# Optimization experiments

Measured on AMD Instinct MI355X. Metric: run time of the kernel, lower is better.

Reference implementation:

```python
import jax, jax.numpy as jnp
import numpy as np

B, T, S, H = 8, 256, 256, 512

def setup_inputs() -> dict:
    key = jax.random.key(0)
    k1, k2, k3, k4, k5, k6 = jax.random.split(key, 6)
    query = jax.random.normal(k1, (B, T, H), dtype=jnp.float32)
    encoder_outputs = jax.random.normal(k2, (B, S, H), dtype=jnp.float32)
    # lengths in [1, S] so every row has at least one valid source position
    src_lengths = jax.random.randint(k3, (B,), 1, S + 1, dtype=jnp.int64)
    scale = 1.0 / np.sqrt(H)
    W_h = jax.random.normal(k4, (H, H), dtype=jnp.float32) * scale  # nn.Linear weight (out, in)
    W_s = jax.random.normal(k5, (H, H), dtype=jnp.float32) * scale
    v = jax.random.normal(k6, (H,), dtype=jnp.float32) * scale     # nn.Linear(H,1) weight squeezed
    return {"query": query, "encoder_outputs": encoder_outputs,
            "src_lengths": src_lengths, "W_h": W_h, "W_s": W_s, "v": v}

def reference(query, encoder_outputs, src_lengths, W_h, W_s, v):
    # Linear without bias: y = x @ W^T
    enc_f = jnp.einsum('bsh,oh->bso', encoder_outputs, W_h)   # (B,S,H)
    qry_f = jnp.einsum('bth,oh->bto', query, W_s)             # (B,T,H)
    # additive score: v^T tanh(enc_f + qry_f), broadcast over (T,S)
    scores = jnp.einsum('btsh,h->bts',
                        jnp.tanh(enc_f[:, None, :, :] + qry_f[:, :, None, :]), v)  # (B,T,S)
    mask = jnp.arange(S)[None, :] >= src_lengths[:, None]      # (B,S) True = pad
    scores = jnp.where(mask[:, None, :], -jnp.inf, scores)
    attn_weights = jax.nn.softmax(scores, axis=-1)             # (B,T,S)
    attn_out = jnp.einsum('bts,bsh->bth', attn_weights, encoder_outputs)
    return attn_out
```

## Files before the change

### kernel.cpp

```cpp
#include <hip/hip_runtime.h>
#include <cstddef>
#include <math.h>

#define BD 8
#define TD 256
#define SD 256
#define HD 512
#define K2F 2.885390081777927f

#define EXP2(x) __builtin_amdgcn_exp2f(x)
#define RCP(x)  __builtin_amdgcn_rcpf(x)

typedef __attribute__((ext_vector_type(8))) short short8;
typedef __attribute__((ext_vector_type(4))) float float4v;
typedef unsigned short u16;

__device__ __forceinline__ u16 bf_hi(float x) {
    union { float f; unsigned u; } v; v.f = x;
    unsigned r = v.u + 0x7fff + ((v.u >> 16) & 1);
    return (u16)(r >> 16);
}
__device__ __forceinline__ float bf_tof(u16 h) {
    union { float f; unsigned u; } v; v.u = ((unsigned)h) << 16;
    return v.f;
}
__device__ __forceinline__ float exp2_sat(float x) {
    return EXP2(fminf(fmaxf(x, -80.0f), 80.0f));
}

__global__ __launch_bounds__(256) void convert_kernel(
    const float* __restrict__ enc, const float* __restrict__ qry,
    const float* __restrict__ Wh,  const float* __restrict__ Ws,
    u16* __restrict__ Ah, u16* __restrict__ Al,
    u16* __restrict__ Bh, u16* __restrict__ Bl)
{
    const int bid = blockIdx.x, tid = threadIdx.x;
    const float* src; u16 *dh, *dl; size_t i4;
    if (bid < 1024)      { src = enc; dh = Ah;                    dl = Al;                    i4 = (size_t)bid * 256 + tid; }
    else if (bid < 2048) { src = qry; dh = Ah + (size_t)2048*512; dl = Al + (size_t)2048*512; i4 = (size_t)(bid-1024)*256 + tid; }
    else if (bid < 2304) { src = Wh;  dh = Bh;                    dl = Bl;                    i4 = (size_t)(bid-2048)*256 + tid; }
    else                 { src = Ws;  dh = Bh + (size_t)512*512;  dl = Bl + (size_t)512*512;  i4 = (size_t)(bid-2304)*256 + tid; }
    float4 x = ((const float4*)src)[i4];
    u16 h0 = bf_hi(x.x), h1 = bf_hi(x.y), h2 = bf_hi(x.z), h3 = bf_hi(x.w);
    ushort4 hv = make_ushort4(h0, h1, h2, h3);
    ushort4 lv = make_ushort4(bf_hi(x.x - bf_tof(h0)), bf_hi(x.y - bf_tof(h1)),
                              bf_hi(x.z - bf_tof(h2)), bf_hi(x.w - bf_tof(h3)));
    ((ushort4*)dh)[i4] = hv;
    ((ushort4*)dl)[i4] = lv;
}

#define LSTR 40
__global__ __launch_bounds__(256) void proj_kernel(
    const u16* __restrict__ Ahg, const u16* __restrict__ Alg,
    const u16* __restrict__ Bhg, const u16* __restrict__ Blg,
    float* __restrict__ encT, float* __restrict__ qryf)
{
    __shared__ u16 LAh[64*LSTR], LAl[64*LSTR], LBh[64*LSTR], LBl[64*LSTR];

    const int tid = threadIdx.x;
    const int l = tid & 63, w = tid >> 6;
    const int rf = l & 15, q = l >> 4;
    const int my = blockIdx.y;
    const bool isq = my >= 32;
    const int m0 = my * 64;
    const int n0 = blockIdx.x * 64;
    const int brow0 = (isq ? 512 : 0) + n0;

    const int srow = tid >> 2;
    const int scol = (tid & 3) * 8;
    const u16* pAh = Ahg + (size_t)(m0 + srow) * HD + scol;
    const u16* pAl = Alg + (size_t)(m0 + srow) * HD + scol;
    const u16* pBh = Bhg + (size_t)(brow0 + srow) * HD + scol;
    const u16* pBl = Blg + (size_t)(brow0 + srow) * HD + scol;

    const int mi = (w & 1) * 32, ni = (w >> 1) * 32;

    float4v acc[2][2] = {{{0,0,0,0},{0,0,0,0}},{{0,0,0,0},{0,0,0,0}}};

    short8 rah = *(const short8*)pAh;
    short8 ral = *(const short8*)pAl;
    short8 rbh = *(const short8*)pBh;
    short8 rbl = *(const short8*)pBl;

    for (int ks = 0; ks < 16; ++ks) {
        if (ks) __syncthreads();
        *(short8*)&LAh[srow * LSTR + scol] = rah;
        *(short8*)&LAl[srow * LSTR + scol] = ral;
        *(short8*)&LBh[srow * LSTR + scol] = rbh;
        *(short8*)&LBl[srow * LSTR + scol] = rbl;
        __syncthreads();
        if (ks + 1 < 16) {
            const int ko = (ks + 1) * 32;
            rah = *(const short8*)(pAh + ko);
            ral = *(const short8*)(pAl + ko);
            rbh = *(const short8*)(pBh + ko);
            rbl = *(const short8*)(pBl + ko);
        }
        short8 ah[2], al[2], bh[2], bl[2];
        #pragma unroll
        for (int i = 0; i < 2; ++i) {
            ah[i] = *(const short8*)&LAh[(mi + i * 16 + rf) * LSTR + q * 8];
            al[i] = *(const short8*)&LAl[(mi + i * 16 + rf) * LSTR + q * 8];
            bh[i] = *(const short8*)&LBh[(ni + i * 16 + rf) * LSTR + q * 8];
            bl[i] = *(const short8*)&LBl[(ni + i * 16 + rf) * LSTR + q * 8];
        }
        #pragma unroll
        for (int i = 0; i < 2; ++i)
            #pragma unroll
            for (int j = 0; j < 2; ++j) {
                acc[i][j] = __builtin_amdgcn_mfma_f32_16x16x32_bf16(ah[i], bh[j], acc[i][j], 0, 0, 0);
                acc[i][j] = __builtin_amdgcn_mfma_f32_16x16x32_bf16(ah[i], bl[j], acc[i][j], 0, 0, 0);
                acc[i][j] = __builtin_amdgcn_mfma_f32_16x16x32_bf16(al[i], bh[j], acc[i][j], 0, 0, 0);
            }
    }

    if (!isq) {
        const int b  = m0 >> 8;
        const int sb = (m0 & 255) + mi + q * 4;
        float* base = encT + (size_t)b * HD * SD;
        #pragma unroll
        for (int i = 0; i < 2; ++i)
            #pragma unroll
            for (int j = 0; j < 2; ++j) {
                float4 o = make_float4(exp2_sat(acc[i][j][0]*K2F), exp2_sat(acc[i][j][1]*K2F),
                                       exp2_sat(acc[i][j][2]*K2F), exp2_sat(acc[i][j][3]*K2F));
                *(float4*)(base + (size_t)(n0 + ni + j * 16 + rf) * SD + sb + i * 16) = o;
            }
    } else {
        const int mrow = (m0 - 2048) + mi + q * 4;
        #pragma unroll
        for (int i = 0; i < 2; ++i)
            #pragma unroll
            for (int j = 0; j < 2; ++j)
                #pragma unroll
                for (int r = 0; r < 4; ++r)
                    qryf[(size_t)(mrow + i * 16 + r) * HD + n0 + ni + j * 16 + rf] =
                        exp2_sat(acc[i][j][r] * K2F);
    }
}

__global__ __launch_bounds__(512) void attn_kernel(
    const float* __restrict__ enc,
    const float* __restrict__ encT,
    const float* __restrict__ qry_f,
    const float* __restrict__ v,
    const int*   __restrict__ lens,
    float* __restrict__ out)
{
    __shared__ float qls[HD * 4];
    __shared__ float pls[8 * 4 * 256];
    __shared__ float wls[4 * SD];

    const int blk = blockIdx.x;
    const int b   = blk >> 6;
    const int t0  = (blk & 63) * 4;
    const int tid = threadIdx.x;
    const int w   = tid >> 6;
    const int l   = tid & 63;

    {
        const float* qf = qry_f + ((size_t)b * TD + t0) * HD;
        float4 qv;
        qv.x = qf[0 * HD + tid]; qv.y = qf[1 * HD + tid];
        qv.z = qf[2 * HD + tid]; qv.w = qf[3 * HD + tid];
        *(float4*)&qls[tid * 4] = qv;
    }
    __syncthreads();

    float a[4][4];
    #pragma unroll
    for (int t = 0; t < 4; ++t)
        #pragma unroll
        for (int c = 0; c < 4; ++c) a[t][c] = 0.0f;
    {
        const float* ep = encT + (size_t)b * HD * SD + (size_t)(w * 64) * SD + l * 4;
        const int jbase = w * 64;
        #pragma unroll 4
        for (int jj = 0; jj < 64; ++jj) {
            float4 e = *(const float4*)(ep + (size_t)jj * SD);
            float4 q4 = *(const float4*)&qls[(jbase + jj) * 4];
            float vj = v[jbase + jj];
            float ev[4] = {e.x, e.y, e.z, e.w};
            float qv[4] = {q4.x, q4.y, q4.z, q4.w};
            #pragma unroll
            for (int t = 0; t < 4; ++t)
                #pragma unroll
                for (int c = 0; c < 4; ++c) {
                    float p = fmaf(ev[c], qv[t], 1.0f);
                    a[t][c] = fmaf(vj, RCP(p), a[t][c]);
                }
        }
    }
    #pragma unroll
    for (int t = 0; t < 4; ++t)
        *(float4*)&pls[(w * 4 + t) * 256 + l * 4] = make_float4(a[t][0], a[t][1], a[t][2], a[t][3]);
    __syncthreads();

    if (w < 4) {
        const int t = w;
        float p[4] = {0, 0, 0, 0};
        #pragma unroll
        for (int g = 0; g < 8; ++g) {
            float4 pp = *(const float4*)&pls[(g * 4 + t) * 256 + l * 4];
            p[0] += pp.x; p[1] += pp.y; p[2] += pp.z; p[3] += pp.w;
        }
        const int len = lens[b];
        const int s0 = l * 4;
        float sc[4];
        #pragma unroll
        for (int c = 0; c < 4; ++c)
            sc[c] = (s0 + c < len) ? -2.0f * p[c] : -INFINITY;
        float mx = fmaxf(fmaxf(sc[0], sc[1]), fmaxf(sc[2], sc[3]));
        #pragma unroll
        for (int off = 32; off; off >>= 1) mx = fmaxf(mx, __shfl_xor(mx, off));
        float ex[4]; float sum = 0.0f;
        #pragma unroll
        for (int c = 0; c < 4; ++c) { ex[c] = __expf(sc[c] - mx); sum += ex[c]; }
        #pragma unroll
        for (int off = 32; off; off >>= 1) sum += __shfl_xor(sum, off);
        const float inv = RCP(sum);
        *(float4*)&wls[t * SD + s0] = make_float4(ex[0]*inv, ex[1]*inv, ex[2]*inv, ex[3]*inv);
    }
    __syncthreads();

    const int g  = tid >> 7;
    const int h4 = (tid & 127) * 4;
    float* avred = pls;
    {
        const float* eb = enc + (size_t)b * SD * HD + h4;
        float4 o[4] = {{0,0,0,0},{0,0,0,0},{0,0,0,0},{0,0,0,0}};
        #pragma unroll 2
        for (int ss = 0; ss < 64; ++ss) {
            const int s = g * 64 + ss;
            float4 evv = *(const float4*)(eb + (size_t)s * HD);
            float wt[4];
            #pragma unroll
            for (int t = 0; t < 4; ++t) wt[t] = wls[t * SD + s];
            #pragma unroll
            for (int t = 0; t < 4; ++t) {
                o[t].x = fmaf(wt[t], evv.x, o[t].x);
                o[t].y = fmaf(wt[t], evv.y, o[t].y);
                o[t].z = fmaf(wt[t], evv.z, o[t].z);
                o[t].w = fmaf(wt[t], evv.w, o[t].w);
            }
        }
        #pragma unroll
        for (int t = 0; t < 4; ++t)
            *(float4*)&avred[(size_t)(g * 4 + t) * 512 + h4] = o[t];
    }
    __syncthreads();

    {
        const int t  = tid >> 7;
        const int hh = (tid & 127) * 4;
        float4 r = {0, 0, 0, 0};
        #pragma unroll
        for (int gg = 0; gg < 4; ++gg) {
            float4 x = *(const float4*)&avred[(size_t)(gg * 4 + t) * 512 + hh];
            r.x += x.x; r.y += x.y; r.z += x.z; r.w += x.w;
        }
        *(float4*)(out + ((size_t)b * TD + t0 + t) * HD + hh) = r;
    }
}

extern "C" void kernel_launch(void* const* d_in, const int* in_sizes, int n_in,
                              void* d_out, int out_size, void* d_ws, size_t ws_size,
                              hipStream_t stream) {
    const float* query = (const float*)d_in[0];
    const float* enc   = (const float*)d_in[1];
    const int*   lens  = (const int*)d_in[2];
    const float* W_h   = (const float*)d_in[3];
    const float* W_s   = (const float*)d_in[4];
    const float* v     = (const float*)d_in[5];
    float* out = (float*)d_out;

    char* ws = (char*)d_ws;
    float* encT = (float*)(ws);
    float* qryf = (float*)(ws + ((size_t)4  << 20));
    u16*   Ah   = (u16*)  (ws + ((size_t)8  << 20));
    u16*   Al   = (u16*)  (ws + ((size_t)12 << 20));
    u16*   Bh   = (u16*)  (ws + ((size_t)16 << 20));
    u16*   Bl   = (u16*)  (ws + ((size_t)17 << 20));

    convert_kernel<<<2560, 256, 0, stream>>>(enc, query, W_h, W_s, Ah, Al, Bh, Bl);

    dim3 pgrid(HD / 64, 64);
    proj_kernel<<<pgrid, 256, 0, stream>>>(Ah, Al, Bh, Bl, encT, qryf);

    attn_kernel<<<BD * (TD / 4), 512, 0, stream>>>(enc, encT, qryf, v, lens, out);
}
```

Baseline: 128.8 us.

## Replace split-bf16 projection with single fp16 MFMA and fuse conversion into GEMM

Drops the separate convert kernel and the hi/lo bf16 split: the projection GEMM now loads fp32 inputs directly, converts them to fp16 in registers and runs one f16 MFMA per tile instead of three bf16 MFMAs. This removes a kernel launch, the workspace round trip and two thirds of the MFMA work. The cost is lower precision, since fp16 has an 11-bit mantissa versus roughly 16 bits for the hi/lo split, and fp16 has limited range. The attention loop also software-prefetches the next encT row and changes its unroll, which reads one row past the end of each 64-row slice.

```diff
diff --git a/kernel.cpp b/kernel.cpp
--- a/kernel.cpp
+++ b/kernel.cpp
@@ -11,51 +11,20 @@
 #define EXP2(x) __builtin_amdgcn_exp2f(x)
 #define RCP(x)  __builtin_amdgcn_rcpf(x)
 
-typedef __attribute__((ext_vector_type(8))) short short8;
+typedef __attribute__((ext_vector_type(8))) _Float16 half8;
 typedef __attribute__((ext_vector_type(4))) float float4v;
-typedef unsigned short u16;
-
-__device__ __forceinline__ u16 bf_hi(float x) {
-    union { float f; unsigned u; } v; v.f = x;
-    unsigned r = v.u + 0x7fff + ((v.u >> 16) & 1);
-    return (u16)(r >> 16);
-}
-__device__ __forceinline__ float bf_tof(u16 h) {
-    union { float f; unsigned u; } v; v.u = ((unsigned)h) << 16;
-    return v.f;
-}
+
 __device__ __forceinline__ float exp2_sat(float x) {
     return EXP2(fminf(fmaxf(x, -80.0f), 80.0f));
 }
 
-__global__ __launch_bounds__(256) void convert_kernel(
+#define LSTR 40
+__global__ __launch_bounds__(256) void proj_kernel(
     const float* __restrict__ enc, const float* __restrict__ qry,
     const float* __restrict__ Wh,  const float* __restrict__ Ws,
-    u16* __restrict__ Ah, u16* __restrict__ Al,
-    u16* __restrict__ Bh, u16* __restrict__ Bl)
-{
-    const int bid = blockIdx.x, tid = threadIdx.x;
-    const float* src; u16 *dh, *dl; size_t i4;
-    if (bid < 1024)      { src = enc; dh = Ah;                    dl = Al;                    i4 = (size_t)bid * 256 + tid; }
-    else if (bid < 2048) { src = qry; dh = Ah + (size_t)2048*512; dl = Al + (size_t)2048*512; i4 = (size_t)(bid-1024)*256 + tid; }
-    else if (bid < 2304) { src = Wh;  dh = Bh;                    dl = Bl;                    i4 = (size_t)(bid-2048)*256 + tid; }
-    else                 { src = Ws;  dh = Bh + (size_t)512*512;  dl = Bl + (size_t)512*512;  i4 = (size_t)(bid-2304)*256 + tid; }
-    float4 x = ((const float4*)src)[i4];
-    u16 h0 = bf_hi(x.x), h1 = bf_hi(x.y), h2 = bf_hi(x.z), h3 = bf_hi(x.w);
-    ushort4 hv = make_ushort4(h0, h1, h2, h3);
-    ushort4 lv = make_ushort4(bf_hi(x.x - bf_tof(h0)), bf_hi(x.y - bf_tof(h1)),
-                              bf_hi(x.z - bf_tof(h2)), bf_hi(x.w - bf_tof(h3)));
-    ((ushort4*)dh)[i4] = hv;
-    ((ushort4*)dl)[i4] = lv;
-}
-
-#define LSTR 40
-__global__ __launch_bounds__(256) void proj_kernel(
-    const u16* __restrict__ Ahg, const u16* __restrict__ Alg,
-    const u16* __restrict__ Bhg, const u16* __restrict__ Blg,
     float* __restrict__ encT, float* __restrict__ qryf)
 {
-    __shared__ u16 LAh[64*LSTR], LAl[64*LSTR], LBh[64*LSTR], LBl[64*LSTR];
+    __shared__ _Float16 LA[64 * LSTR], LB[64 * LSTR];
 
     const int tid = threadIdx.x;
     const int l = tid & 63, w = tid >> 6;
@@ -64,54 +33,53 @@
     const bool isq = my >= 32;
     const int m0 = my * 64;
     const int n0 = blockIdx.x * 64;
-    const int brow0 = (isq ? 512 : 0) + n0;
 
     const int srow = tid >> 2;
     const int scol = (tid & 3) * 8;
-    const u16* pAh = Ahg + (size_t)(m0 + srow) * HD + scol;
-    const u16* pAl = Alg + (size_t)(m0 + srow) * HD + scol;
-    const u16* pBh = Bhg + (size_t)(brow0 + srow) * HD + scol;
-    const u16* pBl = Blg + (size_t)(brow0 + srow) * HD + scol;
+    const float* Abase = isq
+        ? qry + (size_t)(m0 - 2048 + srow) * HD + scol
+        : enc + (size_t)(m0 + srow) * HD + scol;
+    const float* Bbase = (isq ? Ws : Wh) + (size_t)(n0 + srow) * HD + scol;
 
     const int mi = (w & 1) * 32, ni = (w >> 1) * 32;
 
     float4v acc[2][2] = {{{0,0,0,0},{0,0,0,0}},{{0,0,0,0},{0,0,0,0}}};
 
-    short8 rah = *(const short8*)pAh;
-    short8 ral = *(const short8*)pAl;
-    short8 rbh = *(const short8*)pBh;
-    short8 rbl = *(const short8*)pBl;
+    float4 a0 = *(const float4*)(Abase);
+    float4 a1 = *(const float4*)(Abase + 4);
+    float4 b0 = *(const float4*)(Bbase);
+    float4 b1 = *(const float4*)(Bbase + 4);
 
     for (int ks = 0; ks < 16; ++ks) {
         if (ks) __syncthreads();
-        *(short8*)&LAh[srow * LSTR + scol] = rah;
-        *(short8*)&LAl[srow * LSTR + scol] = ral;
-        *(short8*)&LBh[srow * LSTR + scol] = rbh;
-        *(short8*)&LBl[srow * LSTR + scol] = rbl;
+        {
+            float af[8] = {a0.x,a0.y,a0.z,a0.w,a1.x,a1.y,a1.z,a1.w};
+            float bf[8] = {b0.x,b0.y,b0.z,b0.w,b1.x,b1.y,b1.z,b1.w};
+            half8 ha, hb;
+            #pragma unroll
+            for (int i = 0; i < 8; ++i) { ha[i] = (_Float16)af[i]; hb[i] = (_Float16)bf[i]; }
+            *(half8*)&LA[srow * LSTR + scol] = ha;
+            *(half8*)&LB[srow * LSTR + scol] = hb;
+        }
         __syncthreads();
         if (ks + 1 < 16) {
             const int ko = (ks + 1) * 32;
-            rah = *(const short8*)(pAh + ko);
-            ral = *(const short8*)(pAl + ko);
-            rbh = *(const short8*)(pBh + ko);
-            rbl = *(const short8*)(pBl + ko);
-        }
-        short8 ah[2], al[2], bh[2], bl[2];
+            a0 = *(const float4*)(Abase + ko);
+            a1 = *(const float4*)(Abase + ko + 4);
+            b0 = *(const float4*)(Bbase + ko);
+            b1 = *(const float4*)(Bbase + ko + 4);
+        }
+        half8 ah[2], bh[2];
         #pragma unroll
         for (int i = 0; i < 2; ++i) {
-            ah[i] = *(const short8*)&LAh[(mi + i * 16 + rf) * LSTR + q * 8];
-            al[i] = *(const short8*)&LAl[(mi + i * 16 + rf) * LSTR + q * 8];
-            bh[i] = *(const short8*)&LBh[(ni + i * 16 + rf) * LSTR + q * 8];
-            bl[i] = *(const short8*)&LBl[(ni + i * 16 + rf) * LSTR + q * 8];
+            ah[i] = *(const half8*)&LA[(mi + i * 16 + rf) * LSTR + q * 8];
+            bh[i] = *(const half8*)&LB[(ni + i * 16 + rf) * LSTR + q * 8];
         }
         #pragma unroll
         for (int i = 0; i < 2; ++i)
             #pragma unroll
-            for (int j = 0; j < 2; ++j) {
-                acc[i][j] = __builtin_amdgcn_mfma_f32_16x16x32_bf16(ah[i], bh[j], acc[i][j], 0, 0, 0);
-                acc[i][j] = __builtin_amdgcn_mfma_f32_16x16x32_bf16(ah[i], bl[j], acc[i][j], 0, 0, 0);
-                acc[i][j] = __builtin_amdgcn_mfma_f32_16x16x32_bf16(al[i], bh[j], acc[i][j], 0, 0, 0);
-            }
+            for (int j = 0; j < 2; ++j)
+                acc[i][j] = __builtin_amdgcn_mfma_f32_16x16x32_f16(ah[i], bh[j], acc[i][j], 0, 0, 0);
     }
 
     if (!isq) {
@@ -175,9 +143,10 @@
     {
         const float* ep = encT + (size_t)b * HD * SD + (size_t)(w * 64) * SD + l * 4;
         const int jbase = w * 64;
-        #pragma unroll 4
+        float4 e = *(const float4*)ep;
+        #pragma unroll 2
         for (int jj = 0; jj < 64; ++jj) {
-            float4 e = *(const float4*)(ep + (size_t)jj * SD);
+            float4 en = *(const float4*)(ep + (size_t)(jj + 1) * SD);
             float4 q4 = *(const float4*)&qls[(jbase + jj) * 4];
             float vj = v[jbase + jj];
             float ev[4] = {e.x, e.y, e.z, e.w};
@@ -189,6 +158,7 @@
                     float p = fmaf(ev[c], qv[t], 1.0f);
                     a[t][c] = fmaf(vj, RCP(p), a[t][c]);
                 }
+            e = en;
         }
     }
     #pragma unroll
@@ -276,16 +246,10 @@
 
     char* ws = (char*)d_ws;
     float* encT = (float*)(ws);
-    float* qryf = (float*)(ws + ((size_t)4  << 20));
-    u16*   Ah   = (u16*)  (ws + ((size_t)8  << 20));
-    u16*   Al   = (u16*)  (ws + ((size_t)12 << 20));
-    u16*   Bh   = (u16*)  (ws + ((size_t)16 << 20));
-    u16*   Bl   = (u16*)  (ws + ((size_t)17 << 20));
-
-    convert_kernel<<<2560, 256, 0, stream>>>(enc, query, W_h, W_s, Ah, Al, Bh, Bl);
+    float* qryf = (float*)(ws + ((size_t)4 << 20));
 
     dim3 pgrid(HD / 64, 64);
-    proj_kernel<<<pgrid, 256, 0, stream>>>(Ah, Al, Bh, Bl, encT, qryf);
+    proj_kernel<<<pgrid, 256, 0, stream>>>(enc, query, W_h, W_s, encT, qryf);
 
     attn_kernel<<<BD * (TD / 4), 512, 0, stream>>>(enc, encT, qryf, v, lens, out);
 }
```

Result: faster. 124.5 us (-3.3%).
